# Performance work log

Hardware: AMD Instinct MI355X
Metric: run time of the kernel (lower is better)

The kernel has to match this reference:

```python
import jax, jax.numpy as jnp
import numpy as np


def setup_inputs() -> dict:
    key = jax.random.key(0)
    k1, k2, k3, k4 = jax.random.split(key, 4)
    batch, n_channels, t = 4, 2048, 2048
    n_blocks, block_size, ks = 128, 64, 16
    n_block_row = n_channels // block_size  # 32
    x = jax.random.normal(k1, (batch, n_channels, t), dtype=jnp.float32)
    block_values = jax.random.normal(k2, (n_blocks, block_size, block_size, ks), dtype=jnp.float32) * 0.05
    cols = jax.random.randint(k3, (n_blocks,), 0, n_block_row, dtype=jnp.int32)
    rows = jax.random.randint(k4, (n_blocks,), 0, n_block_row, dtype=jnp.int32)
    return {"x": x, "block_values": block_values, "cols": cols, "rows": rows}


def reference(x, block_values, cols, rows):
    # x: (B, C, T); block_values: (n_blocks, bs, bs, ks)
    batch, n_channels, t = x.shape
    n_blocks, bs, _, ks = block_values.shape
    n_block_row = -(-n_channels // bs)
    pad = n_block_row * bs - n_channels
    if pad > 0:
        x = jnp.pad(x, ((0, 0), (0, pad), (0, 0)))
    xb = x.reshape(batch, n_block_row, bs, t)
    # gather active block rows: (B, n_blocks, bs, T) -> (B, n_blocks*bs, T)
    x_unfold = xb[:, cols].reshape(batch, n_blocks * bs, t)
    # grouped causal conv: weights shared across batch, groups = n_blocks
    W = block_values.reshape(n_blocks * bs, bs, ks)  # (O, I/g, K)
    o = jax.lax.conv_general_dilated(
        x_unfold, W,
        window_strides=(1,),
        padding=[(ks - 1, 0)],  # causal: equals padding=ks-1 then [..., :t]
        dimension_numbers=("NCH", "OIH", "NCH"),
        feature_group_count=n_blocks,
    )  # (B, n_blocks*bs, T)
    o = o.reshape(batch, n_blocks, bs, t)
    # scatter-add block outputs into their target block rows
    y = jnp.zeros((batch, n_block_row, bs, t), o.dtype).at[:, rows].add(o)
    y = y.reshape(batch, n_block_row * bs, t)
    return y[:, :n_channels, :]
```

## Files before the change

kernel.cpp:

```cpp
#include <hip/hip_runtime.h>
#include <hip/hip_bf16.h>
#include <stdint.h>

typedef __bf16 bf16_t;
typedef bf16_t bf16x8 __attribute__((ext_vector_type(8)));
typedef float f32x4 __attribute__((ext_vector_type(4)));

#define T_LEN 2048
#define C_LEN 2048
#define NB 128
#define TN 256
#define SROWS 2064
#define XROWS 288

#define GLL(gp, lp) __builtin_amdgcn_global_load_lds( \
    (const __attribute__((address_space(1))) uint32_t*)(gp), \
    (__attribute__((address_space(3))) uint32_t*)(lp), 16, 0, 0)

__global__ __launch_bounds__(256) void prepack_kernel(
    const float* __restrict__ bv, bf16_t* __restrict__ wpk)
{
  const int blk = blockIdx.x;
  const int mt  = blockIdx.y;
  const int tid = threadIdx.x;
  __shared__ float lw[16 * 64 * 17];

  const float* src = bv + (size_t)blk * 65536 + (size_t)mt * 16384;
  for (int p = 0; p < 16; ++p) {
    int idx = p * 1024 + tid * 4;
    const float4 v = *(const float4*)(src + idx);
    int o = idx >> 10;
    int i = (idx >> 4) & 63;
    int k = idx & 15;
    float* d = &lw[(o * 64 + i) * 17 + k];
    d[0] = v.x; d[1] = v.y; d[2] = v.z; d[3] = v.w;
  }
  __syncthreads();

  const int e0 = tid * 2;
  const int l  = e0 >> 3;
  const int j  = e0 & 7;
  const int o  = l & 15;
  for (int ks = 0; ks < 32; ++ks) {
    const int k  = ks >> 1;
    const int i0 = (ks & 1) * 32 + (l >> 4) * 8 + j;
    const float a = lw[(o * 64 + i0) * 17 + k];
    const float b = lw[(o * 64 + i0 + 1) * 17 + k];
    const uint16_t ba = __builtin_bit_cast(uint16_t, (bf16_t)a);
    const uint16_t bb = __builtin_bit_cast(uint16_t, (bf16_t)b);
    const uint32_t packed = (uint32_t)ba | ((uint32_t)bb << 16);
    const size_t off = ((((size_t)blk * 32 + ks) * 4 + mt) * 512) + e0;
    *(uint32_t*)(wpk + off) = packed;
  }
}

__global__ __launch_bounds__(256) void padzero_kernel(bf16_t* __restrict__ S)
{
  const int p = blockIdx.x;
  const size_t g = (p < 64) ? ((size_t)(p >> 4) * SROWS + (p & 15))
                            : ((size_t)4 * SROWS + (p - 64));
  uint4 z = {0u, 0u, 0u, 0u};
  *(uint4*)(S + g * C_LEN + (size_t)threadIdx.x * 8) = z;
}

__global__ __launch_bounds__(256) void xprep_kernel(
    const float* __restrict__ x, bf16_t* __restrict__ S)
{
  const int tb = blockIdx.x, cb = blockIdx.y, n = blockIdx.z;
  const int tid = threadIdx.x;
  __shared__ float lt[64 * 67 + 4];

  #pragma unroll
  for (int p = 0; p < 4; ++p) {
    const int idx = p * 256 + tid;
    const int c   = idx >> 4;
    const int t4  = (idx & 15) * 4;
    const float4 v = *(const float4*)(
        x + ((size_t)n * C_LEN + cb * 64 + c) * T_LEN + tb * 64 + t4);
    float* d = &lt[c * 67 + t4];
    d[0] = v.x; d[1] = v.y; d[2] = v.z; d[3] = v.w;
  }
  __syncthreads();

  #pragma unroll
  for (int p = 0; p < 2; ++p) {
    const int idx = p * 256 + tid;
    const int tl  = idx >> 3;
    const int seg = idx & 7;
    const int t   = tb * 64 + tl;
    const int cbase = (seg * 8) ^ ((t & 7) << 3);
    uint32_t w[4];
    #pragma unroll
    for (int h = 0; h < 4; ++h) {
      const float a = lt[(cbase + 2 * h) * 67 + tl];
      const float b = lt[(cbase + 2 * h + 1) * 67 + tl];
      const uint16_t ba = __builtin_bit_cast(uint16_t, (bf16_t)a);
      const uint16_t bb = __builtin_bit_cast(uint16_t, (bf16_t)b);
      w[h] = (uint32_t)ba | ((uint32_t)bb << 16);
    }
    uint4 u4 = {w[0], w[1], w[2], w[3]};
    *(uint4*)(S + ((size_t)n * SROWS + 16 + t) * C_LEN + cb * 64 + seg * 8) = u4;
  }
}

__global__ __launch_bounds__(256, 2) void bsconv_kernel(
    const bf16_t* __restrict__ S, const bf16_t* __restrict__ wpk,
    const int* __restrict__ cols, const int* __restrict__ rows,
    float* __restrict__ y)
{
  const int tt = blockIdx.x, tr = blockIdx.y, n = blockIdx.z;
  const int t0 = tt * TN;
  const int tid = threadIdx.x;
  const int lane = tid & 63, wv = tid >> 6;

  __shared__ __attribute__((aligned(16))) bf16_t xst[XROWS * 64];
  __shared__ __attribute__((aligned(16))) bf16_t wlds[2][4096];
  __shared__ int alist[NB];
  __shared__ unsigned long long wmask[2];

  {
    const int r  = (tid < NB) ? rows[tid] : -1;
    const int cb = (tid < NB) ? cols[tid] : 0;
    const bool match = (r == tr);
    const unsigned long long m = __ballot(match);
    if (wv < 2 && lane == 0) wmask[wv] = m;
    __syncthreads();
    if (match) {
      int pos = __popcll(wmask[wv] & ((1ull << lane) - 1ull));
      if (wv == 1) pos += __popcll(wmask[0]);
      alist[pos] = tid | (cb << 8);
    }
    __syncthreads();
  }
  const int cnt = __popcll(wmask[0]) + __popcll(wmask[1]);

  f32x4 acc[4][4];
  #pragma unroll
  for (int a = 0; a < 4; ++a)
    #pragma unroll
    for (int b = 0; b < 4; ++b) {
      f32x4 z = {0.f, 0.f, 0.f, 0.f};
      acc[a][b] = z;
    }

  const size_t srow0 = (size_t)n * SROWS + t0;
  const int lxb = tid * 16;

  auto issue_x = [&](int cb) {
    #pragma unroll
    for (int q = 0; q < 9; ++q) {
      const int lb = q * 4096 + lxb;
      const int u  = lb >> 7;
      const int ib = (lb >> 1) & 63;
      GLL(S + (srow0 + u) * C_LEN + cb * 64 + ib, (char*)xst + lb);
    }
  };
  auto issue_w = [&](const bf16_t* wblk, int c, int buf) {
    const bf16_t* wsrc = wblk + (size_t)c * 4096;
    #pragma unroll
    for (int p = 0; p < 2; ++p) {
      const int lb = p * 4096 + lxb;
      GLL(wsrc + (lb >> 1), (char*)wlds[buf] + lb);
    }
  };

  if (cnt > 0) {
    issue_x(alist[0] >> 8);
    issue_w(wpk + (size_t)(alist[0] & 255) * 65536, 0, 0);
  }

  for (int j = 0; j < cnt; ++j) {
    const bf16_t* wblk = wpk + (size_t)(alist[j] & 255) * 65536;
    const bool havenext = (j + 1 < cnt);
    const int anext = havenext ? alist[j + 1] : 0;

    #pragma unroll
    for (int c = 0; c < 16; ++c) {
      if (c < 15) {
        issue_w(wblk, c + 1, (c + 1) & 1);
      } else if (havenext) {
        issue_w(wpk + (size_t)(anext & 255) * 65536, 0, 0);
      }

      if (c < 15 || havenext) {
        asm volatile("s_waitcnt vmcnt(2)" ::: "memory");
      } else {
        asm volatile("s_waitcnt vmcnt(0)" ::: "memory");
      }
      __builtin_amdgcn_s_barrier();
      __builtin_amdgcn_sched_barrier(0);

      const bf16_t* wl = wlds[c & 1];
      __builtin_amdgcn_s_setprio(1);
      #pragma unroll
      for (int ksl = 0; ksl < 2; ++ksl) {
        const int k  = c;
        const int ih = ksl * 32;
        bf16x8 afr[4];
        #pragma unroll
        for (int mt = 0; mt < 4; ++mt)
          afr[mt] = *(const bf16x8*)(wl + ((ksl * 4 + mt) * 64 + lane) * 8);
        const int ub   = wv * 64 + (lane & 15) + k + 1;
        const int scol = (ih + ((lane >> 4) & 3) * 8) ^ ((ub & 7) << 3);
        bf16x8 bfr[4];
        #pragma unroll
        for (int nt = 0; nt < 4; ++nt)
          bfr[nt] = *(const bf16x8*)(xst + (ub + nt * 16) * 64 + scol);
        #pragma unroll
        for (int mt = 0; mt < 4; ++mt)
          #pragma unroll
          for (int nt = 0; nt < 4; ++nt)
            acc[mt][nt] = __builtin_amdgcn_mfma_f32_16x16x32_bf16(
                afr[mt], bfr[nt], acc[mt][nt], 0, 0, 0);
      }
      __builtin_amdgcn_s_setprio(0);
      __builtin_amdgcn_sched_barrier(0);
      __builtin_amdgcn_s_barrier();
    }

    if (havenext) issue_x(anext >> 8);
  }

  const int mlo = ((lane >> 4) & 3) * 4, nn = lane & 15;
  #pragma unroll
  for (int mt = 0; mt < 4; ++mt) {
    #pragma unroll
    for (int nt = 0; nt < 4; ++nt) {
      const int t = t0 + wv * 64 + nt * 16 + nn;
      float* yp = y + ((size_t)n * C_LEN + (size_t)(tr * 64 + mt * 16 + mlo)) * T_LEN + t;
      #pragma unroll
      for (int r = 0; r < 4; ++r)
        yp[(size_t)r * T_LEN] = acc[mt][nt][r];
    }
  }
}

extern "C" void kernel_launch(void* const* d_in, const int* in_sizes, int n_in,
                              void* d_out, int out_size, void* d_ws, size_t ws_size,
                              hipStream_t stream) {
  const float* x   = (const float*)d_in[0];
  const float* bv  = (const float*)d_in[1];
  const int* cols  = (const int*)d_in[2];
  const int* rows  = (const int*)d_in[3];
  float* y = (float*)d_out;

  bf16_t* wpk = (bf16_t*)d_ws;
  bf16_t* S   = (bf16_t*)((char*)d_ws + 16777216);

  prepack_kernel<<<dim3(128, 4), dim3(256), 0, stream>>>(bv, wpk);
  padzero_kernel<<<dim3(80), dim3(256), 0, stream>>>(S);
  xprep_kernel<<<dim3(32, 32, 4), dim3(256), 0, stream>>>(x, S);
  bsconv_kernel<<<dim3(8, 32, 4), dim3(256), 0, stream>>>(S, wpk, cols, rows, y);
}
```

Measured before the change: 185.6 us.

## Double time tile to 512 and stage four taps of weights per barrier

Widens each workgroup to 512 threads covering 512 time steps, so every staged input tile feeds twice as many outputs. Weight staging now moves four kernel taps (eight k-slices) per double-buffered stage instead of one, cutting barriers and wait points per active block from 16 to 4. The input tile load clamps its row index to the end of the padded buffer. In exchange the kernel uses about 137 KB of LDS and runs one workgroup per CU, which lowers occupancy and halves the grid, with possible load imbalance across block rows.

```diff
diff --git a/kernel.cpp b/kernel.cpp
--- a/kernel.cpp
+++ b/kernel.cpp
@@ -9,9 +9,10 @@
 #define T_LEN 2048
 #define C_LEN 2048
 #define NB 128
-#define TN 256
+#define TN 512
 #define SROWS 2064
-#define XROWS 288
+#define XROWS 576
+#define SLAST 8271
 
 #define GLL(gp, lp) __builtin_amdgcn_global_load_lds( \
     (const __attribute__((address_space(1))) uint32_t*)(gp), \
@@ -103,7 +104,7 @@
   }
 }
 
-__global__ __launch_bounds__(256, 2) void bsconv_kernel(
+__global__ __launch_bounds__(512, 1) void bsconv_kernel(
     const bf16_t* __restrict__ S, const bf16_t* __restrict__ wpk,
     const int* __restrict__ cols, const int* __restrict__ rows,
     float* __restrict__ y)
@@ -114,7 +115,7 @@
   const int lane = tid & 63, wv = tid >> 6;
 
   __shared__ __attribute__((aligned(16))) bf16_t xst[XROWS * 64];
-  __shared__ __attribute__((aligned(16))) bf16_t wlds[2][4096];
+  __shared__ __attribute__((aligned(16))) bf16_t wlds[2][16384];
   __shared__ int alist[NB];
   __shared__ unsigned long long wmask[2];
 
@@ -149,24 +150,25 @@
   auto issue_x = [&](int cb) {
     #pragma unroll
     for (int q = 0; q < 9; ++q) {
-      const int lb = q * 4096 + lxb;
-      const int u  = lb >> 7;
+      const int lb = q * 8192 + lxb;
+      size_t gr = srow0 + (size_t)(lb >> 7);
+      if (gr > (size_t)SLAST) gr = (size_t)SLAST;
       const int ib = (lb >> 1) & 63;
-      GLL(S + (srow0 + u) * C_LEN + cb * 64 + ib, (char*)xst + lb);
+      GLL(S + gr * C_LEN + cb * 64 + ib, (char*)xst + lb);
     }
   };
   auto issue_w = [&](const bf16_t* wblk, int c, int buf) {
-    const bf16_t* wsrc = wblk + (size_t)c * 4096;
-    #pragma unroll
-    for (int p = 0; p < 2; ++p) {
-      const int lb = p * 4096 + lxb;
+    const bf16_t* wsrc = wblk + (size_t)c * 16384;
+    #pragma unroll
+    for (int p = 0; p < 4; ++p) {
+      const int lb = p * 8192 + lxb;
       GLL(wsrc + (lb >> 1), (char*)wlds[buf] + lb);
     }
   };
 
   if (cnt > 0) {
+    issue_w(wpk + (size_t)(alist[0] & 255) * 65536, 0, 0);
     issue_x(alist[0] >> 8);
-    issue_w(wpk + (size_t)(alist[0] & 255) * 65536, 0, 0);
   }
 
   for (int j = 0; j < cnt; ++j) {
@@ -175,50 +177,46 @@
     const int anext = havenext ? alist[j + 1] : 0;
 
     #pragma unroll
-    for (int c = 0; c < 16; ++c) {
-      if (c < 15) {
-        issue_w(wblk, c + 1, (c + 1) & 1);
-      } else if (havenext) {
-        issue_w(wpk + (size_t)(anext & 255) * 65536, 0, 0);
-      }
-
-      if (c < 15 || havenext) {
-        asm volatile("s_waitcnt vmcnt(2)" ::: "memory");
-      } else {
-        asm volatile("s_waitcnt vmcnt(0)" ::: "memory");
-      }
+    for (int s = 0; s < 4; ++s) {
+      if (s < 3) issue_w(wblk, s + 1, (s + 1) & 1);
+      if (s < 3) asm volatile("s_waitcnt vmcnt(4)" ::: "memory");
+      else       asm volatile("s_waitcnt vmcnt(0)" ::: "memory");
       __builtin_amdgcn_s_barrier();
       __builtin_amdgcn_sched_barrier(0);
 
-      const bf16_t* wl = wlds[c & 1];
-      __builtin_amdgcn_s_setprio(1);
+      const bf16_t* wl = wlds[s & 1];
       #pragma unroll
-      for (int ksl = 0; ksl < 2; ++ksl) {
-        const int k  = c;
-        const int ih = ksl * 32;
+      for (int sl = 0; sl < 8; ++sl) {
+        const int su = s * 8 + sl;
+        const int k  = su >> 1;
+        const int ih = (su & 1) * 32;
         bf16x8 afr[4];
         #pragma unroll
         for (int mt = 0; mt < 4; ++mt)
-          afr[mt] = *(const bf16x8*)(wl + ((ksl * 4 + mt) * 64 + lane) * 8);
+          afr[mt] = *(const bf16x8*)(wl + ((sl * 4 + mt) * 64 + lane) * 8);
         const int ub   = wv * 64 + (lane & 15) + k + 1;
         const int scol = (ih + ((lane >> 4) & 3) * 8) ^ ((ub & 7) << 3);
         bf16x8 bfr[4];
         #pragma unroll
         for (int nt = 0; nt < 4; ++nt)
           bfr[nt] = *(const bf16x8*)(xst + (ub + nt * 16) * 64 + scol);
+        __builtin_amdgcn_s_setprio(1);
         #pragma unroll
         for (int mt = 0; mt < 4; ++mt)
           #pragma unroll
           for (int nt = 0; nt < 4; ++nt)
             acc[mt][nt] = __builtin_amdgcn_mfma_f32_16x16x32_bf16(
                 afr[mt], bfr[nt], acc[mt][nt], 0, 0, 0);
+        __builtin_amdgcn_s_setprio(0);
       }
-      __builtin_amdgcn_s_setprio(0);
       __builtin_amdgcn_sched_barrier(0);
       __builtin_amdgcn_s_barrier();
     }
 
-    if (havenext) issue_x(anext >> 8);
+    if (havenext) {
+      issue_w(wpk + (size_t)(anext & 255) * 65536, 0, 0);
+      issue_x(anext >> 8);
+    }
   }
 
   const int mlo = ((lane >> 4) & 3) * 4, nn = lane & 15;
@@ -250,5 +248,5 @@
   prepack_kernel<<<dim3(128, 4), dim3(256), 0, stream>>>(bv, wpk);
   padzero_kernel<<<dim3(80), dim3(256), 0, stream>>>(S);
   xprep_kernel<<<dim3(32, 32, 4), dim3(256), 0, stream>>>(x, S);
-  bsconv_kernel<<<dim3(8, 32, 4), dim3(256), 0, stream>>>(S, wpk, cols, rows, y);
-}
+  bsconv_kernel<<<dim3(4, 32, 4), dim3(512), 0, stream>>>(S, wpk, cols, rows, y);
+}
```

Result: no change. 188.9 us (+1.8%).
